# Kernel tuning notes

Hardware: AMD Instinct MI355X
Metric: run time of the kernel (lower is better)

## Reference

```python
import jax, jax.numpy as jnp
import numpy as np
import math

B, L, S, H, E, D = 4, 2048, 2048, 8, 64, 64


def setup_inputs() -> dict:
    key = jax.random.key(0)
    kq, kk, kv = jax.random.split(key, 3)
    queries = jax.random.normal(kq, (B, L, H, E), dtype=jnp.float32)
    keys = jax.random.normal(kk, (B, S, H, E), dtype=jnp.float32)
    values = jax.random.normal(kv, (B, S, H, D), dtype=jnp.float32)
    # TriangularCausalMask: True above the diagonal = masked out
    attn_mask = jnp.triu(jnp.ones((L, S), dtype=bool), k=1)[None, None]  # [1,1,L,S]
    return {"queries": queries, "keys": keys, "values": values, "attn_mask": attn_mask}


def reference(queries, keys, values, attn_mask):
    # queries [B,L,H,E], keys [B,S,H,E], values [B,S,H,D], attn_mask bool [1,1,L,S]
    scale = 1.0 / math.sqrt(queries.shape[-1])
    scores = jnp.einsum('blhe,bshe->bhls', queries, keys)  # [B,H,L,S]
    scores = jnp.where(attn_mask, -jnp.inf, scores)
    A = jax.nn.softmax(scale * scores, axis=-1)  # dropout p=0.0 -> identity
    V = jnp.einsum('bhls,bshd->blhd', A, values)  # [B,L,H,D]
    return V
```

## Files before the change

### kernel.cpp

```cpp
#include <hip/hip_runtime.h>


typedef unsigned short u16;
typedef unsigned int   u32;
typedef short short8   __attribute__((ext_vector_type(8)));
typedef float floatx16 __attribute__((ext_vector_type(16)));
typedef u32 u32x4      __attribute__((ext_vector_type(4)));

#define B_ 4
#define L_ 2048
#define S_ 2048
#define H_ 8
#define E_ 64
#define D_ 64

static __device__ __forceinline__ u32 pack2(float lo, float hi) {
    const u32 a = __float_as_uint(lo) + 0x8000u;
    const u32 b = __float_as_uint(hi) + 0x8000u;
    return __builtin_amdgcn_perm(b, a, 0x07060302u);
}
static __device__ __forceinline__ u16 bf16c(float x) {
    return (u16)((__float_as_uint(x) + 0x8000u) >> 16);
}
static __device__ __forceinline__ void pl32swap(u32& a, u32& b) {
    asm("v_permlane32_swap_b32 %0, %1" : "+v"(a), "+v"(b));
}
static __device__ __forceinline__ floatx16 zero16() {
    floatx16 z;
    #pragma unroll
    for (int i = 0; i < 16; i++) z[i] = 0.f;
    return z;
}

__global__ __launch_bounds__(256)
void cvt_kernel(const float* __restrict__ k, const float* __restrict__ v,
                u16* __restrict__ kc, u16* __restrict__ vt)
{
    __shared__ u16 Lt[64 * 72];
    const int bx = blockIdx.x, t = threadIdx.x;
    if (bx < 2048) {
        const size_t f = ((size_t)bx * 256 + t) * 8;
        const int e0 = (int)(f & 63);
        const int h  = (int)((f >> 6) & 7);
        const int s  = (int)((f >> 9) & 2047);
        const int b  = (int)(f >> 20);
        const float4* kp = (const float4*)(k + f);
        const float4 a0 = kp[0], a1 = kp[1];
        const u32x4 wv = {pack2(a0.x, a0.y), pack2(a0.z, a0.w),
                          pack2(a1.x, a1.y), pack2(a1.z, a1.w)};
        *(u32x4*)&kc[((size_t)(b * 8 + h) * 2048 + s) * 64 + e0] = wv;
    } else {
        const int vb = bx - 2048;
        const int st = vb & 31, h = (vb >> 5) & 7, b = vb >> 8;
        const int s0 = st * 64;
        {
            const int i  = t >> 2;
            const int d0 = (t & 3) * 16;
            const float4* vp = (const float4*)(v + (((size_t)(b * 2048 + s0 + i)) * 8 + h) * 64 + d0);
            const float4 a0 = vp[0], a1 = vp[1], a2 = vp[2], a3 = vp[3];
            const float va[16] = {a0.x,a0.y,a0.z,a0.w, a1.x,a1.y,a1.z,a1.w,
                                  a2.x,a2.y,a2.z,a2.w, a3.x,a3.y,a3.z,a3.w};
            #pragma unroll
            for (int jj = 0; jj < 16; jj++) Lt[(d0 + jj) * 72 + i] = bf16c(va[jj]);
        }
        __syncthreads();
        {
            const int d  = t >> 2;
            const int i0 = (t & 3) * 16;
            const u32x4 w0 = *(const u32x4*)&Lt[d * 72 + i0];
            const u32x4 w1 = *(const u32x4*)&Lt[d * 72 + i0 + 8];
            u16* dst = &vt[(((size_t)(b * 8 + h)) * 64 + d) * 2048 + s0 + i0];
            *(u32x4*)dst = w0;
            *(u32x4*)&dst[8] = w1;
        }
    }
}

template<int SRC>
__global__ __launch_bounds__(128, 2)
void fa_causal32_kernel(const float* __restrict__ q, const float* __restrict__ kk,
                        const float* __restrict__ vv, const u16* __restrict__ kc,
                        const u16* __restrict__ vt, float* __restrict__ out)
{
    const int tid  = threadIdx.x;
    const int w    = tid >> 6;
    const int lane = tid & 63;
    const int l31  = lane & 31;
    const int hi   = lane >> 5;

    const int bx = blockIdx.x;
    const int h  = bx & 7;
    const int b  = (bx >> 3) & 3;
    const int j  = bx >> 5;
    const int s32 = w ? (63 - j) : j;
    const int q0  = s32 * 32;
    const int kt_last = s32 >> 1;

    const float kscale = 0.18033688011112042f;

    const float* qptr = q + (((size_t)b * L_ + q0 + l31) * H_ + h) * E_ + hi * 8;
    short8 qf[4];
    #pragma unroll
    for (int ks = 0; ks < 4; ks++) {
        const float4 a0 = *(const float4*)(qptr + ks * 16);
        const float4 a1 = *(const float4*)(qptr + ks * 16 + 4);
        const u32x4 u = {pack2(a0.x * kscale, a0.y * kscale), pack2(a0.z * kscale, a0.w * kscale),
                         pack2(a1.x * kscale, a1.y * kscale), pack2(a1.z * kscale, a1.w * kscale)};
        qf[ks] = __builtin_bit_cast(short8, u);
    }

    const size_t bh = (size_t)(b * 8 + h);
    const u16* kcb = kc + bh * 2048 * 64;
    const u16* vtb = vt + bh * 64 * 2048;

    auto loadK = [&](int kt, int mt, int ks) -> short8 {
        if constexpr (SRC == 0) {
            const u32x4 u = *(const u32x4*)&kcb[((size_t)(kt * 64 + mt * 32 + l31)) * 64 + ks * 16 + hi * 8];
            return __builtin_bit_cast(short8, u);
        } else {
            const float* p = kk + (((size_t)b * S_ + kt * 64 + mt * 32 + l31) * H_ + h) * E_ + ks * 16 + hi * 8;
            const float4 a0 = *(const float4*)p;
            const float4 a1 = *(const float4*)(p + 4);
            const u32x4 u = {pack2(a0.x, a0.y), pack2(a0.z, a0.w), pack2(a1.x, a1.y), pack2(a1.z, a1.w)};
            return __builtin_bit_cast(short8, u);
        }
    };
    auto loadV = [&](int kt, int nt, int ks) -> short8 {
        if constexpr (SRC == 0) {
            const u32x4 u = *(const u32x4*)&vtb[((size_t)(nt * 32 + l31)) * 2048 + kt * 64 + ks * 16 + hi * 8];
            return __builtin_bit_cast(short8, u);
        } else {
            float f[8];
            #pragma unroll
            for (int jj = 0; jj < 8; jj++)
                f[jj] = vv[(((size_t)b * S_ + kt * 64 + ks * 16 + hi * 8 + jj) * H_ + h) * D_ + nt * 32 + l31];
            const u32x4 u = {pack2(f[0], f[1]), pack2(f[2], f[3]), pack2(f[4], f[5]), pack2(f[6], f[7])};
            return __builtin_bit_cast(short8, u);
        }
    };

    floatx16 occ[2] = {zero16(), zero16()};
    float m_run = -1e30f, l_run = 0.f;

    short8 kf[2][4], vf[2][4];
    #pragma unroll
    for (int mt = 0; mt < 2; mt++)
        #pragma unroll
        for (int ks = 0; ks < 4; ks++) { kf[mt][ks] = loadK(0, mt, ks); vf[mt][ks] = loadV(0, mt, ks); }

    for (int kt = 0; kt <= kt_last; kt++) {
        floatx16 sac[2];
        __builtin_amdgcn_s_setprio(1);
        #pragma unroll
        for (int mt = 0; mt < 2; mt++) {
            floatx16 c = zero16();
            #pragma unroll
            for (int ks = 0; ks < 4; ks++)
                c = __builtin_amdgcn_mfma_f32_32x32x16_bf16(kf[mt][ks], qf[ks], c, 0, 0, 0);
            sac[mt] = c;
        }
        __builtin_amdgcn_s_setprio(0);

        if (kt < kt_last) {
            #pragma unroll
            for (int mt = 0; mt < 2; mt++)
                #pragma unroll
                for (int ks = 0; ks < 4; ks++) kf[mt][ks] = loadK(kt + 1, mt, ks);
        }

        if (kt == kt_last) {
            const int qg = q0 + l31;
            #pragma unroll
            for (int mt = 0; mt < 2; mt++)
                #pragma unroll
                for (int r = 0; r < 16; r++) {
                    const int keyg = kt * 64 + mt * 32 + (r & 3) + (r >> 2) * 8 + hi * 4;
                    if (keyg > qg) sac[mt][r] = -1e30f;
                }
        }

        float red[16];
        #pragma unroll
        for (int r = 0; r < 16; r++) red[r] = fmaxf(sac[0][r], sac[1][r]);
        #pragma unroll
        for (int stp = 8; stp > 0; stp >>= 1)
            #pragma unroll
            for (int r = 0; r < stp; r++) red[r] = fmaxf(red[r], red[r + stp]);
        const float mx   = fmaxf(red[0], __shfl_xor(red[0], 32));
        const float mnew = fmaxf(m_run, mx);
        const float alpha = exp2f(m_run - mnew);
        m_run = mnew;

        float sum[16];
        #pragma unroll
        for (int r = 0; r < 16; r++) {
            sac[0][r] = exp2f(sac[0][r] - mnew);
            sac[1][r] = exp2f(sac[1][r] - mnew);
            sum[r] = sac[0][r] + sac[1][r];
        }
        #pragma unroll
        for (int stp = 8; stp > 0; stp >>= 1)
            #pragma unroll
            for (int r = 0; r < stp; r++) sum[r] += sum[r + stp];
        const float ps = sum[0] + __shfl_xor(sum[0], 32);
        l_run = l_run * alpha + ps;

        #pragma unroll
        for (int nt = 0; nt < 2; nt++)
            #pragma unroll
            for (int r = 0; r < 16; r++) occ[nt][r] *= alpha;

        u32 pk0[8], pk1[8];
        #pragma unroll
        for (int r2 = 0; r2 < 4; r2++) {
            pk0[r2 * 2 + 0] = pack2(sac[0][4 * r2 + 0], sac[0][4 * r2 + 1]);
            pk0[r2 * 2 + 1] = pack2(sac[0][4 * r2 + 2], sac[0][4 * r2 + 3]);
            pk1[r2 * 2 + 0] = pack2(sac[1][4 * r2 + 0], sac[1][4 * r2 + 1]);
            pk1[r2 * 2 + 1] = pack2(sac[1][4 * r2 + 2], sac[1][4 * r2 + 3]);
        }

        __builtin_amdgcn_s_setprio(1);
        #pragma unroll
        for (int ks = 0; ks < 4; ks++) {
            const int u = (ks & 1) * 4;
            u32 w0, w1, w2, w3;
            if (ks < 2) { w0 = pk0[u]; w1 = pk0[u + 1]; w2 = pk0[u + 2]; w3 = pk0[u + 3]; }
            else        { w0 = pk1[u]; w1 = pk1[u + 1]; w2 = pk1[u + 2]; w3 = pk1[u + 3]; }
            pl32swap(w0, w2);
            pl32swap(w1, w3);
            const u32x4 pw = {w0, w1, w2, w3};
            const short8 pf = __builtin_bit_cast(short8, pw);
            occ[0] = __builtin_amdgcn_mfma_f32_32x32x16_bf16(vf[0][ks], pf, occ[0], 0, 0, 0);
            occ[1] = __builtin_amdgcn_mfma_f32_32x32x16_bf16(vf[1][ks], pf, occ[1], 0, 0, 0);
        }
        __builtin_amdgcn_s_setprio(0);

        if (kt < kt_last) {
            #pragma unroll
            for (int nt = 0; nt < 2; nt++)
                #pragma unroll
                for (int ks = 0; ks < 4; ks++) vf[nt][ks] = loadV(kt + 1, nt, ks);
        }
    }

    const float inv = 1.0f / l_run;
    float* op = out + (((size_t)b * L_ + q0 + l31) * H_ + h) * D_;
    #pragma unroll
    for (int nt = 0; nt < 2; nt++)
        #pragma unroll
        for (int r2 = 0; r2 < 4; r2++) {
            const float4 o = {occ[nt][4 * r2 + 0] * inv, occ[nt][4 * r2 + 1] * inv,
                              occ[nt][4 * r2 + 2] * inv, occ[nt][4 * r2 + 3] * inv};
            *(float4*)(op + nt * 32 + r2 * 8 + hi * 4) = o;
        }
}

extern "C" void kernel_launch(void* const* d_in, const int* in_sizes, int n_in,
                              void* d_out, int out_size, void* d_ws, size_t ws_size,
                              hipStream_t stream) {
    const float* q = (const float*)d_in[0];
    const float* k = (const float*)d_in[1];
    const float* v = (const float*)d_in[2];
    float* out = (float*)d_out;

    const size_t elems = (size_t)B_ * H_ * S_ * E_;
    const size_t need  = elems * 2 * 2;
    if (d_ws != nullptr && ws_size >= need) {
        u16* kc = (u16*)d_ws;
        u16* vt = kc + elems;
        cvt_kernel<<<dim3(3072), dim3(256), 0, stream>>>(k, v, kc, vt);
        fa_causal32_kernel<0><<<dim3(1024), dim3(128), 0, stream>>>(q, k, v, kc, vt, out);
    } else {
        fa_causal32_kernel<1><<<dim3(1024), dim3(128), 0, stream>>>(q, k, v, nullptr, nullptr, out);
    }
}
```

Before: 172.7 us.

## Split long causal query tiles across two waves, pre-swizzle K/V into MFMA fragment layout

The conversion kernel now writes K and V^T into a per-64-key tile layout that matches the MFMA fragment order, so each lane's fragment load in the attention kernel becomes one contiguous 16-byte read. The attention grid is rebalanced. The 32 longest query tiles of each (b,h) are split across two waves that each take half the key range, and their partial softmax states are merged through shared memory. The remaining short tiles are paired as before. The online-softmax rescale is also skipped when the running max grows by at most 8 (in log2 units), which removes exp and multiply work on most iterations at some risk to range headroom.

```diff
diff --git a/kernel.cpp b/kernel.cpp
--- a/kernel.cpp
+++ b/kernel.cpp
@@ -38,26 +38,32 @@
 {
     __shared__ u16 Lt[64 * 72];
     const int bx = blockIdx.x, t = threadIdx.x;
-    if (bx < 2048) {
-        const size_t f = ((size_t)bx * 256 + t) * 8;
-        const int e0 = (int)(f & 63);
-        const int h  = (int)((f >> 6) & 7);
-        const int s  = (int)((f >> 9) & 2047);
-        const int b  = (int)(f >> 20);
-        const float4* kp = (const float4*)(k + f);
-        const float4 a0 = kp[0], a1 = kp[1];
-        const u32x4 wv = {pack2(a0.x, a0.y), pack2(a0.z, a0.w),
-                          pack2(a1.x, a1.y), pack2(a1.z, a1.w)};
-        *(u32x4*)&kc[((size_t)(b * 8 + h) * 2048 + s) * 64 + e0] = wv;
+    const int tile = bx & 1023;
+    const int kt = tile & 31, h = (tile >> 5) & 7, b = tile >> 8;
+    const int F  = t >> 5;
+    const int hi = (t >> 4) & 1;
+    const int l0 = (t & 15) * 2;
+
+    if (bx < 1024) {
+        const int mt = F >> 2, ks = F & 3;
+        const int s  = kt * 64 + mt * 32 + l0;
+        const int e  = ks * 16 + hi * 8;
+        const float* p0 = k + (((size_t)(b * S_ + s)) * H_ + h) * E_ + e;
+        const float4 a0 = ((const float4*)p0)[0], a1 = ((const float4*)p0)[1];
+        const float* p1 = p0 + H_ * E_;
+        const float4 b0 = ((const float4*)p1)[0], b1 = ((const float4*)p1)[1];
+        u16* dst = kc + ((size_t)(b * 8 + h)) * 131072 + (size_t)kt * 4096 + t * 16;
+        *(u32x4*)dst = (u32x4){pack2(a0.x, a0.y), pack2(a0.z, a0.w),
+                               pack2(a1.x, a1.y), pack2(a1.z, a1.w)};
+        *(u32x4*)(dst + 8) = (u32x4){pack2(b0.x, b0.y), pack2(b0.z, b0.w),
+                                     pack2(b1.x, b1.y), pack2(b1.z, b1.w)};
     } else {
-        const int vb = bx - 2048;
-        const int st = vb & 31, h = (vb >> 5) & 7, b = vb >> 8;
-        const int s0 = st * 64;
         {
             const int i  = t >> 2;
             const int d0 = (t & 3) * 16;
-            const float4* vp = (const float4*)(v + (((size_t)(b * 2048 + s0 + i)) * 8 + h) * 64 + d0);
-            const float4 a0 = vp[0], a1 = vp[1], a2 = vp[2], a3 = vp[3];
+            const float* vp = v + (((size_t)(b * S_ + kt * 64 + i)) * H_ + h) * D_ + d0;
+            const float4 a0 = ((const float4*)vp)[0], a1 = ((const float4*)vp)[1];
+            const float4 a2 = ((const float4*)vp)[2], a3 = ((const float4*)vp)[3];
             const float va[16] = {a0.x,a0.y,a0.z,a0.w, a1.x,a1.y,a1.z,a1.w,
                                   a2.x,a2.y,a2.z,a2.w, a3.x,a3.y,a3.z,a3.w};
             #pragma unroll
@@ -65,23 +71,23 @@
         }
         __syncthreads();
         {
-            const int d  = t >> 2;
-            const int i0 = (t & 3) * 16;
-            const u32x4 w0 = *(const u32x4*)&Lt[d * 72 + i0];
-            const u32x4 w1 = *(const u32x4*)&Lt[d * 72 + i0 + 8];
-            u16* dst = &vt[(((size_t)(b * 8 + h)) * 64 + d) * 2048 + s0 + i0];
-            *(u32x4*)dst = w0;
-            *(u32x4*)&dst[8] = w1;
+            const int nt = F >> 2, ks = F & 3;
+            const int d1 = nt * 32 + l0;
+            u16* dst = vt + ((size_t)(b * 8 + h)) * 131072 + (size_t)kt * 4096 + t * 16;
+            *(u32x4*)dst       = *(const u32x4*)&Lt[(d1    ) * 72 + ks * 16 + hi * 8];
+            *(u32x4*)(dst + 8) = *(const u32x4*)&Lt[(d1 + 1) * 72 + ks * 16 + hi * 8];
         }
     }
 }
 
 template<int SRC>
 __global__ __launch_bounds__(128, 2)
-void fa_causal32_kernel(const float* __restrict__ q, const float* __restrict__ kk,
-                        const float* __restrict__ vv, const u16* __restrict__ kc,
-                        const u16* __restrict__ vt, float* __restrict__ out)
+void fa_kernel(const float* __restrict__ q, const float* __restrict__ kk,
+               const float* __restrict__ vv, const u16* __restrict__ kc,
+               const u16* __restrict__ vt, float* __restrict__ out)
 {
+    __shared__ float Ls[64 * 33 + 128];
+
     const int tid  = threadIdx.x;
     const int w    = tid >> 6;
     const int lane = tid & 63;
@@ -89,12 +95,25 @@
     const int hi   = lane >> 5;
 
     const int bx = blockIdx.x;
-    const int h  = bx & 7;
-    const int b  = (bx >> 3) & 3;
-    const int j  = bx >> 5;
-    const int s32 = w ? (63 - j) : j;
-    const int q0  = s32 * 32;
-    const int kt_last = s32 >> 1;
+    int h, b, s32, kt0, ktend;
+    bool split, diag;
+    if (bx < 1024) {
+        split = true;
+        h = bx & 7; b = (bx >> 3) & 3;
+        s32 = 63 - (bx >> 5);
+        const int klast = s32 >> 1;
+        const int mid   = (klast + 1) >> 1;
+        if (w == 0) { kt0 = 0;   ktend = mid - 1; diag = false; }
+        else        { kt0 = mid; ktend = klast;   diag = true;  }
+    } else {
+        split = false; diag = true;
+        const int idx = bx - 1024;
+        h = idx & 7; b = (idx >> 3) & 3;
+        const int jj = idx >> 5;
+        s32 = w ? jj : (31 - jj);
+        kt0 = 0; ktend = s32 >> 1;
+    }
+    const int q0 = s32 * 32;
 
     const float kscale = 0.18033688011112042f;
 
@@ -110,12 +129,12 @@
     }
 
     const size_t bh = (size_t)(b * 8 + h);
-    const u16* kcb = kc + bh * 2048 * 64;
-    const u16* vtb = vt + bh * 64 * 2048;
+    const u16* kcb = kc + bh * 131072;
+    const u16* vtb = vt + bh * 131072;
 
     auto loadK = [&](int kt, int mt, int ks) -> short8 {
         if constexpr (SRC == 0) {
-            const u32x4 u = *(const u32x4*)&kcb[((size_t)(kt * 64 + mt * 32 + l31)) * 64 + ks * 16 + hi * 8];
+            const u32x4 u = *(const u32x4*)&kcb[(size_t)kt * 4096 + (mt * 4 + ks) * 512 + lane * 8];
             return __builtin_bit_cast(short8, u);
         } else {
             const float* p = kk + (((size_t)b * S_ + kt * 64 + mt * 32 + l31) * H_ + h) * E_ + ks * 16 + hi * 8;
@@ -127,7 +146,7 @@
     };
     auto loadV = [&](int kt, int nt, int ks) -> short8 {
         if constexpr (SRC == 0) {
-            const u32x4 u = *(const u32x4*)&vtb[((size_t)(nt * 32 + l31)) * 2048 + kt * 64 + ks * 16 + hi * 8];
+            const u32x4 u = *(const u32x4*)&vtb[(size_t)kt * 4096 + (nt * 4 + ks) * 512 + lane * 8];
             return __builtin_bit_cast(short8, u);
         } else {
             float f[8];
@@ -146,9 +165,9 @@
     #pragma unroll
     for (int mt = 0; mt < 2; mt++)
         #pragma unroll
-        for (int ks = 0; ks < 4; ks++) { kf[mt][ks] = loadK(0, mt, ks); vf[mt][ks] = loadV(0, mt, ks); }
-
-    for (int kt = 0; kt <= kt_last; kt++) {
+        for (int ks = 0; ks < 4; ks++) { kf[mt][ks] = loadK(kt0, mt, ks); vf[mt][ks] = loadV(kt0, mt, ks); }
+
+    for (int kt = kt0; kt <= ktend; kt++) {
         floatx16 sac[2];
         __builtin_amdgcn_s_setprio(1);
         #pragma unroll
@@ -161,14 +180,14 @@
         }
         __builtin_amdgcn_s_setprio(0);
 
-        if (kt < kt_last) {
+        if (kt < ktend) {
             #pragma unroll
             for (int mt = 0; mt < 2; mt++)
                 #pragma unroll
                 for (int ks = 0; ks < 4; ks++) kf[mt][ks] = loadK(kt + 1, mt, ks);
         }
 
-        if (kt == kt_last) {
+        if (diag && kt == ktend) {
             const int qg = q0 + l31;
             #pragma unroll
             for (int mt = 0; mt < 2; mt++)
@@ -186,29 +205,32 @@
         for (int stp = 8; stp > 0; stp >>= 1)
             #pragma unroll
             for (int r = 0; r < stp; r++) red[r] = fmaxf(red[r], red[r + stp]);
-        const float mx   = fmaxf(red[0], __shfl_xor(red[0], 32));
-        const float mnew = fmaxf(m_run, mx);
-        const float alpha = exp2f(m_run - mnew);
-        m_run = mnew;
+        const float mx = fmaxf(red[0], __shfl_xor(red[0], 32));
+
+        const bool defer = __all(mx - m_run <= 8.0f) != 0;
+        if (!defer) {
+            const float mnew  = fmaxf(m_run, mx);
+            const float alpha = exp2f(m_run - mnew);
+            m_run = mnew;
+            l_run *= alpha;
+            #pragma unroll
+            for (int nt = 0; nt < 2; nt++)
+                #pragma unroll
+                for (int r = 0; r < 16; r++) occ[nt][r] *= alpha;
+        }
 
         float sum[16];
         #pragma unroll
         for (int r = 0; r < 16; r++) {
-            sac[0][r] = exp2f(sac[0][r] - mnew);
-            sac[1][r] = exp2f(sac[1][r] - mnew);
+            sac[0][r] = exp2f(sac[0][r] - m_run);
+            sac[1][r] = exp2f(sac[1][r] - m_run);
             sum[r] = sac[0][r] + sac[1][r];
         }
         #pragma unroll
         for (int stp = 8; stp > 0; stp >>= 1)
             #pragma unroll
             for (int r = 0; r < stp; r++) sum[r] += sum[r + stp];
-        const float ps = sum[0] + __shfl_xor(sum[0], 32);
-        l_run = l_run * alpha + ps;
-
-        #pragma unroll
-        for (int nt = 0; nt < 2; nt++)
-            #pragma unroll
-            for (int r = 0; r < 16; r++) occ[nt][r] *= alpha;
+        l_run += sum[0] + __shfl_xor(sum[0], 32);
 
         u32 pk0[8], pk1[8];
         #pragma unroll
@@ -235,7 +257,7 @@
         }
         __builtin_amdgcn_s_setprio(0);
 
-        if (kt < kt_last) {
+        if (kt < ktend) {
             #pragma unroll
             for (int nt = 0; nt < 2; nt++)
                 #pragma unroll
@@ -243,16 +265,46 @@
         }
     }
 
-    const float inv = 1.0f / l_run;
-    float* op = out + (((size_t)b * L_ + q0 + l31) * H_ + h) * D_;
-    #pragma unroll
-    for (int nt = 0; nt < 2; nt++)
-        #pragma unroll
-        for (int r2 = 0; r2 < 4; r2++) {
-            const float4 o = {occ[nt][4 * r2 + 0] * inv, occ[nt][4 * r2 + 1] * inv,
-                              occ[nt][4 * r2 + 2] * inv, occ[nt][4 * r2 + 3] * inv};
-            *(float4*)(op + nt * 32 + r2 * 8 + hi * 4) = o;
-        }
+    if (split) {
+        if (w == 1) {
+            #pragma unroll
+            for (int nt = 0; nt < 2; nt++)
+                #pragma unroll
+                for (int r = 0; r < 16; r++) Ls[lane * 33 + nt * 16 + r] = occ[nt][r];
+            Ls[2112 + lane] = m_run;
+            Ls[2176 + lane] = l_run;
+        }
+        __syncthreads();
+        if (w == 0) {
+            const float mB = Ls[2112 + lane], lB = Ls[2176 + lane];
+            const float m  = fmaxf(m_run, mB);
+            const float aA = exp2f(m_run - m), aB = exp2f(mB - m);
+            const float inv = 1.0f / (l_run * aA + lB * aB);
+            float* op = out + (((size_t)b * L_ + q0 + l31) * H_ + h) * D_;
+            #pragma unroll
+            for (int nt = 0; nt < 2; nt++)
+                #pragma unroll
+                for (int r2 = 0; r2 < 4; r2++) {
+                    const float4 o = {
+                        (occ[nt][4 * r2 + 0] * aA + Ls[lane * 33 + nt * 16 + 4 * r2 + 0] * aB) * inv,
+                        (occ[nt][4 * r2 + 1] * aA + Ls[lane * 33 + nt * 16 + 4 * r2 + 1] * aB) * inv,
+                        (occ[nt][4 * r2 + 2] * aA + Ls[lane * 33 + nt * 16 + 4 * r2 + 2] * aB) * inv,
+                        (occ[nt][4 * r2 + 3] * aA + Ls[lane * 33 + nt * 16 + 4 * r2 + 3] * aB) * inv};
+                    *(float4*)(op + nt * 32 + r2 * 8 + hi * 4) = o;
+                }
+        }
+    } else {
+        const float inv = 1.0f / l_run;
+        float* op = out + (((size_t)b * L_ + q0 + l31) * H_ + h) * D_;
+        #pragma unroll
+        for (int nt = 0; nt < 2; nt++)
+            #pragma unroll
+            for (int r2 = 0; r2 < 4; r2++) {
+                const float4 o = {occ[nt][4 * r2 + 0] * inv, occ[nt][4 * r2 + 1] * inv,
+                                  occ[nt][4 * r2 + 2] * inv, occ[nt][4 * r2 + 3] * inv};
+                *(float4*)(op + nt * 32 + r2 * 8 + hi * 4) = o;
+            }
+    }
 }
 
 extern "C" void kernel_launch(void* const* d_in, const int* in_sizes, int n_in,
@@ -268,9 +320,9 @@
     if (d_ws != nullptr && ws_size >= need) {
         u16* kc = (u16*)d_ws;
         u16* vt = kc + elems;
-        cvt_kernel<<<dim3(3072), dim3(256), 0, stream>>>(k, v, kc, vt);
-        fa_causal32_kernel<0><<<dim3(1024), dim3(128), 0, stream>>>(q, k, v, kc, vt, out);
+        cvt_kernel<<<dim3(2048), dim3(256), 0, stream>>>(k, v, kc, vt);
+        fa_kernel<0><<<dim3(1536), dim3(128), 0, stream>>>(q, k, v, kc, vt, out);
     } else {
-        fa_causal32_kernel<1><<<dim3(1024), dim3(128), 0, stream>>>(q, k, v, nullptr, nullptr, out);
-    }
-}
+        fa_kernel<1><<<dim3(1536), dim3(128), 0, stream>>>(q, k, v, nullptr, nullptr, out);
+    }
+}
```

Result: faster. 153.4 us (-11.1%).
